# Kernel optimization log

Hardware: AMD Instinct MI355X
Metric: run time of the kernel (lower is better)

Reference implementation:

```python
import jax, jax.numpy as jnp
import numpy as np

MU = 0            # smeared direction (init arg dir)
IS_ODD = False    # init arg is_odd -> update the EVEN subset
DIMS = (24, 24, 24, 24)
N_PLAQ = 6
PI_2 = 0.6366197723675814  # 2/pi, as in scale_coeff


def setup_inputs() -> dict:
    key = jax.random.key(0)
    k1, k2, k3 = jax.random.split(key, 3)
    shape = (4,) + DIMS + (3, 3)  # [dir, T, Z, Y, X, 3, 3]
    x_re = jax.random.normal(k1, shape, jnp.float32)
    x_im = jax.random.normal(k2, shape, jnp.float32)
    coeff = jax.random.uniform(k3, (N_PLAQ,), jnp.float32)
    return {"x_re": x_re, "x_im": x_im, "coeff": coeff}


def _adj(m):
    return jnp.conj(jnp.swapaxes(m, -1, -2))


def _shift(a, nu, n):
    # lattice .shift(nu, n): value at site + n*nu_hat (periodic); lattice axes are the leading 4
    return jnp.roll(a, -n, axis=nu)


def _eo_filter(dims, is_odd, dtype):
    # evenodd_mask % 2; filter is 1 on the UPDATED subset (odd if is_odd else even)
    grids = jnp.meshgrid(*[jnp.arange(d) for d in dims], indexing='ij')
    parity = sum(grids) % 2
    mask = parity if is_odd else 1 - parity
    return mask.astype(dtype)[..., None, None]


def _matexp(Z, terms=12, squarings=4):
    # scaling-and-squaring Taylor (Horner) matrix exponential, batched over leading dims
    Z = Z * jnp.asarray(0.5 ** squarings, dtype=jnp.float32).astype(Z.dtype)
    eye = jnp.eye(Z.shape[-1], dtype=Z.dtype)
    E = eye
    for k in range(terms, 0, -1):
        E = eye + (Z @ E) / k
    for _ in range(squarings):
        E = E @ E
    return E


def reference(x_re, x_im, coeff):
    x = (x_re + 1j * x_im).astype(jnp.complex64)  # [4, T, Z, Y, X, 3, 3]
    filt = _eo_filter(DIMS, IS_ODD, jnp.complex64)
    # filter_fixed_update: mask mu-links; staples built from fixed-subset x[mu]
    xmu_fix = x[MU] * (1.0 - filt)
    xupd = x[MU] * filt
    # scale_coeff(coeff, 0.75) = (2/pi)*0.75*atan(coeff)
    c = (PI_2 * 0.75) * jnp.arctan(coeff)
    cc = c.astype(jnp.complex64)
    # plaquette staples (n_plaq = 6 loops)
    loops = []
    for nu in range(4):
        if nu == MU:
            continue
        Umu = _shift(xmu_fix, nu, 1)      # x[mu].shift(nu, 1)
        Unu = _shift(x[nu], MU, 1)        # x[nu].shift(mu, 1)
        R = Umu @ _adj(Unu)
        stf = x[nu] @ R                   # forward staple
        L = _adj(x[nu]) @ xmu_fix
        stu = L @ Unu
        loops.append(stf)
        loops.append(_shift(stu, nu, -1)) # backward staple
    f = loops[0] * cc[0]
    for i in range(1, N_PLAQ):
        f = f + loops[i] * cc[i]
    f = f / N_PLAQ
    # stout update on the updated subset: Z = projectTangent(f @ xupd^dag); U' = exp(Z) @ U
    M = f @ _adj(xupd)
    A = 0.5 * (M - _adj(M))               # anti-hermitian part
    tr = jnp.trace(A, axis1=-2, axis2=-1)
    Zt = A - (tr / 3.0)[..., None, None] * jnp.eye(3, dtype=A.dtype)  # traceless
    E = _matexp(Zt)
    ymu = E @ xupd + xmu_fix              # combine updated and fixed subsets
    y = x.at[MU].set(ymu)
    # return real/imag stacked so output is real-valued: [4, T, Z, Y, X, 3, 3, 2]
    return jnp.stack((jnp.real(y), jnp.imag(y)), axis=-1)
```

## Files before the change

kernel.cpp:

```cpp
#include <hip/hip_runtime.h>
#include <cstdint>

#define LT 24
#define NSITE (LT*LT*LT*LT)

struct C3 { float re[9]; float im[9]; };

__device__ __forceinline__ void loadM(C3& m, const float* __restrict__ re,
                                      const float* __restrict__ im, int off) {
#pragma unroll
    for (int j = 0; j < 9; ++j) {
        m.re[j] = re[off + j];
        m.im[j] = im[off + j];
    }
}

__device__ __forceinline__ void mmul(C3& o, const C3& a, const C3& b) {
#pragma unroll
    for (int r = 0; r < 3; ++r) {
#pragma unroll
        for (int c = 0; c < 3; ++c) {
            float sr = 0.f, si = 0.f;
#pragma unroll
            for (int k = 0; k < 3; ++k) {
                float ar = a.re[r*3+k], ai = a.im[r*3+k];
                float br = b.re[k*3+c], bi = b.im[k*3+c];
                sr += ar*br - ai*bi;
                si += ar*bi + ai*br;
            }
            o.re[r*3+c] = sr; o.im[r*3+c] = si;
        }
    }
}

__device__ __forceinline__ void mmul_adjB(C3& o, const C3& a, const C3& b) {
#pragma unroll
    for (int r = 0; r < 3; ++r) {
#pragma unroll
        for (int c = 0; c < 3; ++c) {
            float sr = 0.f, si = 0.f;
#pragma unroll
            for (int k = 0; k < 3; ++k) {
                float ar = a.re[r*3+k], ai = a.im[r*3+k];
                float br = b.re[c*3+k], bi = b.im[c*3+k];
                sr += ar*br + ai*bi;
                si += ai*br - ar*bi;
            }
            o.re[r*3+c] = sr; o.im[r*3+c] = si;
        }
    }
}

__device__ __forceinline__ void madjA_mul(C3& o, const C3& a, const C3& b) {
#pragma unroll
    for (int r = 0; r < 3; ++r) {
#pragma unroll
        for (int c = 0; c < 3; ++c) {
            float sr = 0.f, si = 0.f;
#pragma unroll
            for (int k = 0; k < 3; ++k) {
                float ar = a.re[k*3+r], ai = a.im[k*3+r];
                float br = b.re[k*3+c], bi = b.im[k*3+c];
                sr += ar*br + ai*bi;
                si += ar*bi - ai*br;
            }
            o.re[r*3+c] = sr; o.im[r*3+c] = si;
        }
    }
}

__device__ __forceinline__ void macc(C3& f, const C3& s, float cr) {
#pragma unroll
    for (int j = 0; j < 9; ++j) { f.re[j] += cr * s.re[j]; f.im[j] += cr * s.im[j]; }
}

__global__ void interleave_kernel(const float4* __restrict__ re,
                                  const float4* __restrict__ im,
                                  float4* __restrict__ out, int n4) {
    int i = blockIdx.x * blockDim.x + threadIdx.x;
    if (i >= n4) return;
    float4 a = re[i], b = im[i];
    float4 o0, o1;
    o0.x = a.x; o0.y = b.x; o0.z = a.y; o0.w = b.y;
    o1.x = a.z; o1.y = b.z; o1.z = a.w; o1.w = b.w;
    out[2*i]     = o0;
    out[2*i + 1] = o1;
}

__global__ __launch_bounds__(256)
void stout_kernel(const float* __restrict__ xre, const float* __restrict__ xim,
                  const float* __restrict__ coeff, float2* __restrict__ out) {
    int tid = blockIdx.x * blockDim.x + threadIdx.x;
    if (tid >= NSITE / 2) return;

    int xh = tid % 12;  int r0 = tid / 12;
    int y  = r0 % LT;   r0 /= LT;
    int z  = r0 % LT;   int t = r0 / LT;
    int x  = 2 * xh + ((t + z + y) & 1);

    float c[6];
#pragma unroll
    for (int i = 0; i < 6; ++i)
        c[i] = 0.07957747154594768f * atanf(coeff[i]);

    int tp = (t + 1 < LT) ? t + 1 : 0;
    int zp = (z + 1 < LT) ? z + 1 : 0;  int zm = (z > 0) ? z - 1 : LT - 1;
    int yp = (y + 1 < LT) ? y + 1 : 0;  int ym = (y > 0) ? y - 1 : LT - 1;
    int xp = (x + 1 < LT) ? x + 1 : 0;  int xm = (x > 0) ? x - 1 : LT - 1;

    const int s   = ((t  * LT + z) * LT + y) * LT + x;
    const int stt = ((tp * LT + z) * LT + y) * LT + x;
    const int spv[3]  = { ((t  * LT + zp) * LT + y ) * LT + x,
                          ((t  * LT + z ) * LT + yp) * LT + x,
                          ((t  * LT + z ) * LT + y ) * LT + xp };
    const int smv[3]  = { ((t  * LT + zm) * LT + y ) * LT + x,
                          ((t  * LT + z ) * LT + ym) * LT + x,
                          ((t  * LT + z ) * LT + y ) * LT + xm };
    const int smtv[3] = { ((tp * LT + zm) * LT + y ) * LT + x,
                          ((tp * LT + z ) * LT + ym) * LT + x,
                          ((tp * LT + z ) * LT + y ) * LT + xm };

    C3 f;
#pragma unroll
    for (int j = 0; j < 9; ++j) { f.re[j] = 0.f; f.im[j] = 0.f; }

    C3 A, B, Cm, tmp, stp;
#pragma unroll
    for (int i = 0; i < 3; ++i) {
        const int d = i + 1;
        loadM(A,  xre, xim, (d * NSITE + s)      * 9);
        loadM(B,  xre, xim, (     spv[i])        * 9);
        loadM(Cm, xre, xim, (d * NSITE + stt)    * 9);
        mmul_adjB(tmp, B, Cm);
        mmul(stp, A, tmp);
        macc(f, stp, c[2 * i]);
        loadM(A,  xre, xim, (d * NSITE + smv[i]) * 9);
        loadM(B,  xre, xim, (     smv[i])        * 9);
        loadM(Cm, xre, xim, (d * NSITE + smtv[i])* 9);
        madjA_mul(tmp, A, B);
        mmul(stp, tmp, Cm);
        macc(f, stp, c[2 * i + 1]);
    }

    C3 U;
    loadM(U, xre, xim, s * 9);

    C3 Mm;
    mmul_adjB(Mm, f, U);
    C3 Zt;
#pragma unroll
    for (int r = 0; r < 3; ++r) {
#pragma unroll
        for (int cq = 0; cq < 3; ++cq) {
            Zt.re[r*3+cq] = 0.5f * (Mm.re[r*3+cq] - Mm.re[cq*3+r]);
            Zt.im[r*3+cq] = 0.5f * (Mm.im[r*3+cq] + Mm.im[cq*3+r]);
        }
    }
    float trIm = (Zt.im[0] + Zt.im[4] + Zt.im[8]) / 3.0f;
    Zt.im[0] -= trIm; Zt.im[4] -= trIm; Zt.im[8] -= trIm;

#pragma unroll
    for (int j = 0; j < 9; ++j) { Zt.re[j] *= 0.0625f; Zt.im[j] *= 0.0625f; }

    C3 E;
#pragma unroll
    for (int j = 0; j < 9; ++j) { E.re[j] = 0.f; E.im[j] = 0.f; }
    E.re[0] = 1.f; E.re[4] = 1.f; E.re[8] = 1.f;

    C3 Tm;
#pragma unroll
    for (int k = 12; k >= 1; --k) {
        mmul(Tm, Zt, E);
        const float invk = 1.0f / (float)k;
#pragma unroll
        for (int j = 0; j < 9; ++j) {
            E.re[j] = Tm.re[j] * invk;
            E.im[j] = Tm.im[j] * invk;
        }
        E.re[0] += 1.f; E.re[4] += 1.f; E.re[8] += 1.f;
    }
#pragma unroll
    for (int q = 0; q < 4; ++q) {
        mmul(Tm, E, E);
        E = Tm;
    }

    C3 Y;
    mmul(Y, E, U);

    const int ob = s * 9;
#pragma unroll
    for (int j = 0; j < 9; ++j) {
        float2 v; v.x = Y.re[j]; v.y = Y.im[j];
        out[ob + j] = v;
    }
}

extern "C" void kernel_launch(void* const* d_in, const int* in_sizes, int n_in,
                              void* d_out, int out_size, void* d_ws, size_t ws_size,
                              hipStream_t stream) {
    const float* xre   = (const float*)d_in[0];
    const float* xim   = (const float*)d_in[1];
    const float* coeff = (const float*)d_in[2];

    const int n4 = (4 * NSITE * 9) / 4;
    interleave_kernel<<<(n4 + 255) / 256, 256, 0, stream>>>(
        (const float4*)xre, (const float4*)xim, (float4*)d_out, n4);

    stout_kernel<<<(NSITE / 2 + 255) / 256, 256, 0, stream>>>(
        xre, xim, coeff, (float2*)d_out);
}
```

Baseline: 265.4 us.

## Read interleaved complex links from output buffer and fuse staple accumulation

The stout kernel now reads its link matrices from the interleaved re/im copy already written to the output buffer. Each matrix element becomes a single float2 load instead of two loads from separate real and imaginary arrays, which should improve locality of the gathered neighbour loads. The staple product is fused with the coefficient accumulation so the temporary staple matrix is no longer needed, and the interleave kernel now works on float2 inputs per thread. The kernel reads and writes the same buffer while both pointers are marked __restrict__. This relies on writes landing only on even-site mu links while reads of mu links come only from odd neighbours or the thread's own site before its write, and the narrower interleave kernel issues smaller loads and stores.

```diff
diff --git a/kernel.cpp b/kernel.cpp
--- a/kernel.cpp
+++ b/kernel.cpp
@@ -6,12 +6,12 @@
 
 struct C3 { float re[9]; float im[9]; };
 
-__device__ __forceinline__ void loadM(C3& m, const float* __restrict__ re,
-                                      const float* __restrict__ im, int off) {
+__device__ __forceinline__ void loadMi(C3& m, const float2* __restrict__ buf, int site) {
+    const int base = site * 9;
 #pragma unroll
     for (int j = 0; j < 9; ++j) {
-        m.re[j] = re[off + j];
-        m.im[j] = im[off + j];
+        float2 v = buf[base + j];
+        m.re[j] = v.x; m.im[j] = v.y;
     }
 }
 
@@ -33,6 +33,24 @@
     }
 }
 
+__device__ __forceinline__ void mmul_acc(C3& f, const C3& a, const C3& b, float cr) {
+#pragma unroll
+    for (int r = 0; r < 3; ++r) {
+#pragma unroll
+        for (int c = 0; c < 3; ++c) {
+            float sr = 0.f, si = 0.f;
+#pragma unroll
+            for (int k = 0; k < 3; ++k) {
+                float ar = a.re[r*3+k], ai = a.im[r*3+k];
+                float br = b.re[k*3+c], bi = b.im[k*3+c];
+                sr += ar*br - ai*bi;
+                si += ar*bi + ai*br;
+            }
+            f.re[r*3+c] += cr * sr; f.im[r*3+c] += cr * si;
+        }
+    }
+}
+
 __device__ __forceinline__ void mmul_adjB(C3& o, const C3& a, const C3& b) {
 #pragma unroll
     for (int r = 0; r < 3; ++r) {
@@ -69,27 +87,20 @@
     }
 }
 
-__device__ __forceinline__ void macc(C3& f, const C3& s, float cr) {
-#pragma unroll
-    for (int j = 0; j < 9; ++j) { f.re[j] += cr * s.re[j]; f.im[j] += cr * s.im[j]; }
-}
-
-__global__ void interleave_kernel(const float4* __restrict__ re,
-                                  const float4* __restrict__ im,
-                                  float4* __restrict__ out, int n4) {
+__global__ void interleave_kernel(const float2* __restrict__ re,
+                                  const float2* __restrict__ im,
+                                  float4* __restrict__ out, int n2) {
     int i = blockIdx.x * blockDim.x + threadIdx.x;
-    if (i >= n4) return;
-    float4 a = re[i], b = im[i];
-    float4 o0, o1;
-    o0.x = a.x; o0.y = b.x; o0.z = a.y; o0.w = b.y;
-    o1.x = a.z; o1.y = b.z; o1.z = a.w; o1.w = b.w;
-    out[2*i]     = o0;
-    out[2*i + 1] = o1;
+    if (i >= n2) return;
+    float2 a = re[i], b = im[i];
+    float4 o; o.x = a.x; o.y = b.x; o.z = a.y; o.w = b.y;
+    out[i] = o;
 }
 
 __global__ __launch_bounds__(256)
-void stout_kernel(const float* __restrict__ xre, const float* __restrict__ xim,
-                  const float* __restrict__ coeff, float2* __restrict__ out) {
+void stout_kernel(const float2* __restrict__ xi,
+                  const float* __restrict__ coeff,
+                  float2* __restrict__ out) {
     int tid = blockIdx.x * blockDim.x + threadIdx.x;
     if (tid >= NSITE / 2) return;
 
@@ -124,26 +135,24 @@
 #pragma unroll
     for (int j = 0; j < 9; ++j) { f.re[j] = 0.f; f.im[j] = 0.f; }
 
-    C3 A, B, Cm, tmp, stp;
+    C3 A, B, Cm, tmp;
 #pragma unroll
     for (int i = 0; i < 3; ++i) {
         const int d = i + 1;
-        loadM(A,  xre, xim, (d * NSITE + s)      * 9);
-        loadM(B,  xre, xim, (     spv[i])        * 9);
-        loadM(Cm, xre, xim, (d * NSITE + stt)    * 9);
+        loadMi(B,  xi, spv[i]);
+        loadMi(Cm, xi, d * NSITE + stt);
+        loadMi(A,  xi, d * NSITE + s);
         mmul_adjB(tmp, B, Cm);
-        mmul(stp, A, tmp);
-        macc(f, stp, c[2 * i]);
-        loadM(A,  xre, xim, (d * NSITE + smv[i]) * 9);
-        loadM(B,  xre, xim, (     smv[i])        * 9);
-        loadM(Cm, xre, xim, (d * NSITE + smtv[i])* 9);
+        mmul_acc(f, A, tmp, c[2 * i]);
+        loadMi(A,  xi, d * NSITE + smv[i]);
+        loadMi(B,  xi, smv[i]);
+        loadMi(Cm, xi, d * NSITE + smtv[i]);
         madjA_mul(tmp, A, B);
-        mmul(stp, tmp, Cm);
-        macc(f, stp, c[2 * i + 1]);
+        mmul_acc(f, tmp, Cm, c[2 * i + 1]);
     }
 
     C3 U;
-    loadM(U, xre, xim, s * 9);
+    loadMi(U, xi, s);
 
     C3 Mm;
     mmul_adjB(Mm, f, U);
@@ -203,10 +212,10 @@
     const float* xim   = (const float*)d_in[1];
     const float* coeff = (const float*)d_in[2];
 
-    const int n4 = (4 * NSITE * 9) / 4;
-    interleave_kernel<<<(n4 + 255) / 256, 256, 0, stream>>>(
-        (const float4*)xre, (const float4*)xim, (float4*)d_out, n4);
+    const int n2 = (4 * NSITE * 9) / 2;
+    interleave_kernel<<<(n2 + 255) / 256, 256, 0, stream>>>(
+        (const float2*)xre, (const float2*)xim, (float4*)d_out, n2);
 
     stout_kernel<<<(NSITE / 2 + 255) / 256, 256, 0, stream>>>(
-        xre, xim, coeff, (float2*)d_out);
-}
+        (const float2*)d_out, coeff, (float2*)d_out);
+}
```

After: 259.3 us. 2.3% less time.
